# Kernel optimization log

Measured on AMD Instinct MI355X. Metric: run time of the kernel, lower is better.

The kernel has to match this reference:

```python
import math
import jax, jax.numpy as jnp
import numpy as np

B, T, E, H = 4, 2048, 256, 8
OBS_DIM, ACT_DIM = 17, 6
JOINED = OBS_DIM + ACT_DIM + 2  # 25: transition width in TAP trajectory transformer


def setup_inputs() -> dict:
    key = jax.random.key(0)
    ks = jax.random.split(key, 5)
    s = 0.02
    return {
        "x": jax.random.normal(ks[0], (B, T, E), dtype=jnp.float32),
        "Wq": jax.random.normal(ks[1], (E, E), dtype=jnp.float32) * s,
        "bq": jnp.zeros((E,), jnp.float32),
        "Wk": jax.random.normal(ks[2], (E, E), dtype=jnp.float32) * s,
        "bk": jnp.zeros((E,), jnp.float32),
        "Wv": jax.random.normal(ks[3], (E, E), dtype=jnp.float32) * s,
        "bv": jnp.zeros((E,), jnp.float32),
        "Wo": jax.random.normal(ks[4], (E, E), dtype=jnp.float32) * s,
        "bo": jnp.zeros((E,), jnp.float32),
    }


def _mask(t):
    # causal tril with every JOINED-th column (the "done"/boundary token) zeroed
    m = jnp.tril(jnp.ones((t, t), dtype=bool))
    keep_col = (jnp.arange(t) % JOINED) != (JOINED - 1)
    return m & keep_col[None, :]  # (t, t)


def reference(x, Wq, bq, Wk, bk, Wv, bv, Wo, bo):
    b, t, e = x.shape
    d = e // H
    # torch nn.Linear: y = x @ W.T + b
    q = (x @ Wq.T + bq).reshape(b, t, H, d).transpose(0, 2, 1, 3)  # b h t d
    k = (x @ Wk.T + bk).reshape(b, t, H, d).transpose(0, 2, 1, 3)
    v = (x @ Wv.T + bv).reshape(b, t, H, d).transpose(0, 2, 1, 3)

    scores = jnp.einsum("bhtd,bhsd->bhts", q, k) * (1.0 / math.sqrt(d))
    scores = jnp.where(_mask(t)[None, None], scores, -jnp.inf)
    attn = jax.nn.softmax(scores, axis=-1)  # (b, h, t, t) — dropout rate 0 => identity
    out = jnp.einsum("bhts,bhsd->bhtd", attn, v)  # b h t d
    out = out.transpose(0, 2, 1, 3).reshape(b, t, e)  # b t (h d)
    return out @ Wo.T + bo
```

## Files before the change

### kernel.cpp

```cpp
#include <hip/hip_runtime.h>

#define BB 4
#define TT 2048
#define EE 256
#define HH 8
#define DD 32
#define JOINED 25
#define CSCALE 0.2550539239731586f

typedef __attribute__((ext_vector_type(8))) __bf16 bf16x8;
typedef __attribute__((ext_vector_type(4))) float f32x4;

static __device__ __forceinline__ unsigned short f2bf(float f) {
    unsigned u = __float_as_uint(f);
    u += 0x7fffu + ((u >> 16) & 1u);
    return (unsigned short)(u >> 16);
}
static __device__ __forceinline__ unsigned pk2bf(float a, float b) {
    return (unsigned)f2bf(a) | ((unsigned)f2bf(b) << 16);
}

union BF8U { uint4 u; bf16x8 b; };
static __device__ __forceinline__ bf16x8 ld_frag(const unsigned short* p) {
    BF8U t; t.u = *(const uint4*)p; return t.b;
}

#define MFMA(a, b, c) __builtin_amdgcn_mfma_f32_16x16x32_bf16((a), (b), (c), 0, 0, 0)

__global__ __launch_bounds__(256) void prep_kernel(
    const float* __restrict__ x,
    const float* __restrict__ Wq, const float* __restrict__ Wk,
    const float* __restrict__ Wv, const float* __restrict__ Wo,
    unsigned short* __restrict__ xb, unsigned short* __restrict__ wqb,
    unsigned short* __restrict__ wkb, unsigned short* __restrict__ wvb,
    unsigned short* __restrict__ wob, unsigned short* __restrict__ onesG)
{
    const size_t NX = (size_t)BB * TT * EE;
    const size_t NMAIN = NX + 4 * (size_t)EE * EE;
    size_t idx = ((size_t)blockIdx.x * 256 + threadIdx.x) * 8;
    if (idx >= NMAIN) {
        size_t base = idx - NMAIN;
        #pragma unroll
        for (int i = 0; i < 8; ++i) {
            size_t e = base + i;
            if (e < (size_t)JOINED * 64) {
                int phase = (int)(e >> 6), o = (int)(e & 63);
                onesG[e] = (((phase + o) % JOINED) != (JOINED - 1)) ? (unsigned short)0x3F80
                                                                    : (unsigned short)0;
            }
        }
        return;
    }
    const float* src; unsigned short* dst; size_t off;
    if (idx < NX) { src = x; dst = xb; off = idx; }
    else {
        size_t i2 = idx - NX;
        int wsel = (int)(i2 >> 16);
        off = i2 & 65535u;
        src = wsel == 0 ? Wq : wsel == 1 ? Wk : wsel == 2 ? Wv : Wo;
        dst = wsel == 0 ? wqb : wsel == 1 ? wkb : wsel == 2 ? wvb : wob;
    }
    float4 a = *(const float4*)(src + off);
    float4 b = *(const float4*)(src + off + 4);
    uint4 o;
    o.x = pk2bf(a.x, a.y); o.y = pk2bf(a.z, a.w);
    o.z = pk2bf(b.x, b.y); o.w = pk2bf(b.z, b.w);
    *(uint4*)(dst + off) = o;
}

__global__ __launch_bounds__(256) void qkv_kernel(
    const unsigned short* __restrict__ xb,
    const unsigned short* __restrict__ wq, const float* __restrict__ bq,
    const unsigned short* __restrict__ wk, const float* __restrict__ bk,
    const unsigned short* __restrict__ wv, const float* __restrict__ bv,
    unsigned short* __restrict__ qo, unsigned short* __restrict__ ko,
    unsigned short* __restrict__ vto)
{
    __shared__ unsigned short Xs[64*72];
    __shared__ unsigned short Ws[64*72];

    const int m0 = blockIdx.x * 64;
    const int nb = blockIdx.y;
    const int which = nb >> 2;
    const int n0 = (nb & 3) * 64;
    const unsigned short* __restrict__ W = which == 0 ? wq : which == 1 ? wk : wv;
    const float* __restrict__ bias       = which == 0 ? bq : which == 1 ? bk : bv;

    const int tid = threadIdx.x;
    const int w = tid >> 6, lane = tid & 63, quad = lane >> 4, lq = lane & 15;
    const int sr = tid >> 2, sc = (tid & 3) * 16;

    f32x4 acc[4] = {{0,0,0,0},{0,0,0,0},{0,0,0,0},{0,0,0,0}};

    for (int k0 = 0; k0 < EE; k0 += 64) {
        __syncthreads();
        *(uint4*)&Xs[sr*72 + sc]     = *(const uint4*)&xb[(size_t)(m0 + sr)*EE + k0 + sc];
        *(uint4*)&Xs[sr*72 + sc + 8] = *(const uint4*)&xb[(size_t)(m0 + sr)*EE + k0 + sc + 8];
        *(uint4*)&Ws[sr*72 + sc]     = *(const uint4*)&W [(size_t)(n0 + sr)*EE + k0 + sc];
        *(uint4*)&Ws[sr*72 + sc + 8] = *(const uint4*)&W [(size_t)(n0 + sr)*EE + k0 + sc + 8];
        __syncthreads();
        bf16x8 a0 = ld_frag(&Xs[(w*16 + lq)*72 + quad*8]);
        bf16x8 a1 = ld_frag(&Xs[(w*16 + lq)*72 + 32 + quad*8]);
        #pragma unroll
        for (int f = 0; f < 4; ++f) {
            bf16x8 b0 = ld_frag(&Ws[(f*16 + lq)*72 + quad*8]);
            bf16x8 b1 = ld_frag(&Ws[(f*16 + lq)*72 + 32 + quad*8]);
            acc[f] = MFMA(a0, b0, acc[f]);
            acc[f] = MFMA(a1, b1, acc[f]);
        }
    }

    const int t0 = (m0 + w*16 + quad*4);
    const int b  = t0 >> 11;
    const int tl = t0 & (TT - 1);

    #pragma unroll
    for (int f = 0; f < 4; ++f) {
        int n = n0 + f*16 + lq;
        int h = n >> 5, d = n & 31;
        float bb = bias[n];
        if (which == 0) {
            #pragma unroll
            for (int reg = 0; reg < 4; ++reg)
                qo[(((size_t)b*HH + h)*TT + tl + reg)*DD + d] = f2bf((acc[f][reg] + bb) * CSCALE);
        } else if (which == 1) {
            #pragma unroll
            for (int reg = 0; reg < 4; ++reg)
                ko[(((size_t)b*HH + h)*TT + tl + reg)*DD + d] = f2bf(acc[f][reg] + bb);
        } else {
            int r25 = tl % JOINED;
            int mreg = (JOINED - 1) - r25;
            float vv[4];
            #pragma unroll
            for (int reg = 0; reg < 4; ++reg)
                vv[reg] = (reg == mreg) ? 0.f : (acc[f][reg] + bb);
            uint2 pk;
            pk.x = pk2bf(vv[0], vv[1]);
            pk.y = pk2bf(vv[2], vv[3]);
            *(uint2*)&vto[(((size_t)b*HH + h)*DD + d)*TT + tl] = pk;
        }
    }
}

__global__ __launch_bounds__(256, 4) void attn_kernel(
    const unsigned short* __restrict__ q, const unsigned short* __restrict__ k,
    const unsigned short* __restrict__ vt, const unsigned short* __restrict__ onesG,
    unsigned short* __restrict__ ao)
{
    __shared__ unsigned short Ks[2][64*40];
    __shared__ unsigned short Vt[2][32*72];
    __shared__ unsigned short Ps[4][16*72];

    const int L = blockIdx.x;
    const int xcd   = L & 7;
    const int inner = L >> 3;
    const int bh = xcd * 4 + (inner & 3);
    const int iq = 31 - (inner >> 2);
    const int b = bh >> 3, hh = bh & 7;

    const int tid = threadIdx.x;
    const int w = tid >> 6, lane = tid & 63, quad = lane >> 4, lq = lane & 15;
    const int r0 = iq * 64;
    const int q0 = r0 + w*16;
    const int ntiles = iq + 1;

    const int rk = tid >> 2, ck = (tid & 3) * 8;
    const int rv = tid >> 3, cv = (tid & 7) * 8;

    const unsigned short* qb_ = q  + (size_t)bh * TT * DD;
    const unsigned short* kb_ = k  + (size_t)bh * TT * DD;
    const unsigned short* vb_ = vt + (size_t)bh * DD * TT;

    const bf16x8 qf = ld_frag(qb_ + (size_t)(q0 + lq)*DD + quad*8);

    {
        uint4 kreg = *(const uint4*)(kb_ + (size_t)rk*DD + ck);
        uint4 vreg = *(const uint4*)(vb_ + (size_t)rv*TT + cv);
        *(uint4*)&Ks[0][rk*40 + ck] = kreg;
        *(uint4*)&Vt[0][rv*72 + cv] = vreg;
    }
    __syncthreads();

    f32x4 O0 = {0,0,0,0}, O1 = {0,0,0,0}, Ld = {0,0,0,0};
    int phase = 0;

    for (int jt = 0; jt < ntiles; ++jt) {
        const int j0 = jt * 64;
        const int jn = (jt + 1 < ntiles) ? j0 + 64 : j0;
        uint4 kreg = *(const uint4*)(kb_ + (size_t)(jn + rk)*DD + ck);
        uint4 vreg = *(const uint4*)(vb_ + (size_t)rv*TT + jn + cv);

        bf16x8 ones0 = ld_frag(&onesG[phase*64 +      quad*8]);
        bf16x8 ones1 = ld_frag(&onesG[phase*64 + 32 + quad*8]);

        const unsigned short* Kb = &Ks[jt & 1][0];
        const unsigned short* Vb = &Vt[jt & 1][0];

        f32x4 St[4];
        #pragma unroll
        for (int f = 0; f < 4; ++f) {
            bf16x8 kf = ld_frag(&Kb[(f*16 + lq)*40 + quad*8]);
            f32x4 z = {0,0,0,0};
            St[f] = MFMA(kf, qf, z);
        }
        if (jt == ntiles - 1) {
            int row = q0 + lq;
            #pragma unroll
            for (int f = 0; f < 4; ++f) {
                int kvb = j0 + f*16 + quad*4;
                #pragma unroll
                for (int reg = 0; reg < 4; ++reg)
                    St[f][reg] = (kvb + reg <= row) ? St[f][reg] : -1e30f;
            }
        }
        unsigned short* ps = &Ps[w][0];
        #pragma unroll
        for (int f = 0; f < 4; ++f) {
            float p0 = __builtin_amdgcn_exp2f(St[f][0]);
            float p1 = __builtin_amdgcn_exp2f(St[f][1]);
            float p2 = __builtin_amdgcn_exp2f(St[f][2]);
            float p3 = __builtin_amdgcn_exp2f(St[f][3]);
            uint2 pk;
            pk.x = pk2bf(p0, p1);
            pk.y = pk2bf(p2, p3);
            *(uint2*)&ps[lq*72 + f*16 + quad*4] = pk;
        }
        #pragma unroll
        for (int c = 0; c < 2; ++c) {
            bf16x8 pa  = ld_frag(&ps[lq*72 + c*32 + quad*8]);
            bf16x8 v0f = ld_frag(&Vb[(lq)*72      + c*32 + quad*8]);
            bf16x8 v1f = ld_frag(&Vb[(16 + lq)*72 + c*32 + quad*8]);
            O0 = MFMA(pa, v0f, O0);
            O1 = MFMA(pa, v1f, O1);
            Ld = MFMA(pa, (c ? ones1 : ones0), Ld);
        }

        *(uint4*)&Ks[(jt + 1) & 1][rk*40 + ck] = kreg;
        *(uint4*)&Vt[(jt + 1) & 1][rv*72 + cv] = vreg;
        __syncthreads();

        phase += 14; if (phase >= JOINED) phase -= JOINED;
    }

    #pragma unroll
    for (int reg = 0; reg < 4; ++reg) {
        float inv = 1.0f / Ld[reg];
        int t = q0 + quad*4 + reg;
        size_t ob = ((size_t)b*TT + t)*EE + hh*DD;
        ao[ob + lq]      = f2bf(O0[reg] * inv);
        ao[ob + 16 + lq] = f2bf(O1[reg] * inv);
    }
}

__global__ __launch_bounds__(256) void proj_kernel(
    const unsigned short* __restrict__ a, const unsigned short* __restrict__ W,
    const float* __restrict__ bias, float* __restrict__ out)
{
    __shared__ unsigned short Xs[64*72];
    __shared__ unsigned short Ws[64*72];

    const int m0 = blockIdx.x * 64;
    const int n0 = blockIdx.y * 64;
    const int tid = threadIdx.x;
    const int w = tid >> 6, lane = tid & 63, quad = lane >> 4, lq = lane & 15;
    const int sr = tid >> 2, sc = (tid & 3) * 16;

    f32x4 acc[4] = {{0,0,0,0},{0,0,0,0},{0,0,0,0},{0,0,0,0}};

    for (int k0 = 0; k0 < EE; k0 += 64) {
        __syncthreads();
        *(uint4*)&Xs[sr*72 + sc]     = *(const uint4*)&a[(size_t)(m0 + sr)*EE + k0 + sc];
        *(uint4*)&Xs[sr*72 + sc + 8] = *(const uint4*)&a[(size_t)(m0 + sr)*EE + k0 + sc + 8];
        *(uint4*)&Ws[sr*72 + sc]     = *(const uint4*)&W[(size_t)(n0 + sr)*EE + k0 + sc];
        *(uint4*)&Ws[sr*72 + sc + 8] = *(const uint4*)&W[(size_t)(n0 + sr)*EE + k0 + sc + 8];
        __syncthreads();
        bf16x8 a0 = ld_frag(&Xs[(w*16 + lq)*72 + quad*8]);
        bf16x8 a1 = ld_frag(&Xs[(w*16 + lq)*72 + 32 + quad*8]);
        #pragma unroll
        for (int f = 0; f < 4; ++f) {
            bf16x8 b0 = ld_frag(&Ws[(f*16 + lq)*72 + quad*8]);
            bf16x8 b1 = ld_frag(&Ws[(f*16 + lq)*72 + 32 + quad*8]);
            acc[f] = MFMA(a0, b0, acc[f]);
            acc[f] = MFMA(a1, b1, acc[f]);
        }
    }

    #pragma unroll
    for (int f = 0; f < 4; ++f) {
        int n = n0 + f*16 + lq;
        float bb = bias[n];
        #pragma unroll
        for (int reg = 0; reg < 4; ++reg) {
            int m = m0 + w*16 + quad*4 + reg;
            out[(size_t)m*EE + n] = acc[f][reg] + bb;
        }
    }
}

extern "C" void kernel_launch(void* const* d_in, const int* in_sizes, int n_in,
                              void* d_out, int out_size, void* d_ws, size_t ws_size,
                              hipStream_t stream) {
    const float* x  = (const float*)d_in[0];
    const float* Wq = (const float*)d_in[1];
    const float* bq = (const float*)d_in[2];
    const float* Wk = (const float*)d_in[3];
    const float* bk = (const float*)d_in[4];
    const float* Wv = (const float*)d_in[5];
    const float* bv = (const float*)d_in[6];
    const float* Wo = (const float*)d_in[7];
    const float* bo = (const float*)d_in[8];
    float* out = (float*)d_out;

    const size_t n_elem = (size_t)BB * TT * EE;
    const size_t w_elem = (size_t)EE * EE;
    unsigned short* xb    = (unsigned short*)d_ws;
    unsigned short* wqb   = xb  + n_elem;
    unsigned short* wkb   = wqb + w_elem;
    unsigned short* wvb   = wkb + w_elem;
    unsigned short* wob   = wvb + w_elem;
    unsigned short* qq    = wob + w_elem;
    unsigned short* kk    = qq  + n_elem;
    unsigned short* vtt   = kk  + n_elem;
    unsigned short* ao    = vtt + n_elem;
    unsigned short* onesG = ao  + n_elem;

    const int prep_blocks = (int)((n_elem + 4*w_elem) / 2048) + 1;
    prep_kernel<<<dim3(prep_blocks), 256, 0, stream>>>(
        x, Wq, Wk, Wv, Wo, xb, wqb, wkb, wvb, wob, onesG);
    qkv_kernel <<<dim3(BB*TT/64, 12), 256, 0, stream>>>(
        xb, wqb, bq, wkb, bk, wvb, bv, qq, kk, vtt);
    attn_kernel<<<dim3(1024), 256, 0, stream>>>(qq, kk, vtt, onesG, ao);
    proj_kernel<<<dim3(BB*TT/64, EE/64), 256, 0, stream>>>(ao, wob, bo, out);
}
```

Baseline: 120.1 us.

## Use 128-row query tiles with 512-thread blocks and in-LDS ones table

The attention kernel now handles 128 query rows per block with 8 waves. Each K/V tile is loaded into shared memory once and reused by twice as many query rows, and half the threads stage K while the other half stage V. Waves skip key tiles that lie entirely beyond their causal horizon. The boundary-mask ones table is built in LDS inside the attention kernel rather than by prep_kernel in global memory. The cost is fewer blocks, larger blocks, and some idle waves near the causal diagonal.

```diff
diff --git a/kernel.cpp b/kernel.cpp
--- a/kernel.cpp
+++ b/kernel.cpp
@@ -33,24 +33,10 @@
     const float* __restrict__ Wv, const float* __restrict__ Wo,
     unsigned short* __restrict__ xb, unsigned short* __restrict__ wqb,
     unsigned short* __restrict__ wkb, unsigned short* __restrict__ wvb,
-    unsigned short* __restrict__ wob, unsigned short* __restrict__ onesG)
+    unsigned short* __restrict__ wob)
 {
     const size_t NX = (size_t)BB * TT * EE;
-    const size_t NMAIN = NX + 4 * (size_t)EE * EE;
     size_t idx = ((size_t)blockIdx.x * 256 + threadIdx.x) * 8;
-    if (idx >= NMAIN) {
-        size_t base = idx - NMAIN;
-        #pragma unroll
-        for (int i = 0; i < 8; ++i) {
-            size_t e = base + i;
-            if (e < (size_t)JOINED * 64) {
-                int phase = (int)(e >> 6), o = (int)(e & 63);
-                onesG[e] = (((phase + o) % JOINED) != (JOINED - 1)) ? (unsigned short)0x3F80
-                                                                    : (unsigned short)0;
-            }
-        }
-        return;
-    }
     const float* src; unsigned short* dst; size_t off;
     if (idx < NX) { src = x; dst = xb; off = idx; }
     else {
@@ -142,30 +128,38 @@
     }
 }
 
-__global__ __launch_bounds__(256, 4) void attn_kernel(
+__global__ __launch_bounds__(512, 2) void attn_kernel(
     const unsigned short* __restrict__ q, const unsigned short* __restrict__ k,
-    const unsigned short* __restrict__ vt, const unsigned short* __restrict__ onesG,
-    unsigned short* __restrict__ ao)
+    const unsigned short* __restrict__ vt, unsigned short* __restrict__ ao)
 {
     __shared__ unsigned short Ks[2][64*40];
     __shared__ unsigned short Vt[2][32*72];
-    __shared__ unsigned short Ps[4][16*72];
+    __shared__ unsigned short Ps[8][16*72];
+    __shared__ unsigned short onesTab[JOINED*64];
 
     const int L = blockIdx.x;
     const int xcd   = L & 7;
     const int inner = L >> 3;
     const int bh = xcd * 4 + (inner & 3);
-    const int iq = 31 - (inner >> 2);
+    const int iq = 15 - (inner >> 2);
     const int b = bh >> 3, hh = bh & 7;
 
     const int tid = threadIdx.x;
     const int w = tid >> 6, lane = tid & 63, quad = lane >> 4, lq = lane & 15;
-    const int r0 = iq * 64;
+    const int r0 = iq * 128;
     const int q0 = r0 + w*16;
-    const int ntiles = iq + 1;
-
-    const int rk = tid >> 2, ck = (tid & 3) * 8;
-    const int rv = tid >> 3, cv = (tid & 7) * 8;
+    const int ntiles = iq*2 + 2;
+
+    const bool stK = tid < 256;
+    const int t2 = tid & 255;
+    const int rk = t2 >> 2, ck = (t2 & 3) * 8;
+    const int rv = t2 >> 3, cv = (t2 & 7) * 8;
+
+    for (int i = tid; i < JOINED*64; i += 512) {
+        int phase = i >> 6, o = i & 63;
+        onesTab[i] = (((phase + o) % JOINED) != (JOINED - 1)) ? (unsigned short)0x3F80
+                                                              : (unsigned short)0;
+    }
 
     const unsigned short* qb_ = q  + (size_t)bh * TT * DD;
     const unsigned short* kb_ = k  + (size_t)bh * TT * DD;
@@ -173,12 +167,8 @@
 
     const bf16x8 qf = ld_frag(qb_ + (size_t)(q0 + lq)*DD + quad*8);
 
-    {
-        uint4 kreg = *(const uint4*)(kb_ + (size_t)rk*DD + ck);
-        uint4 vreg = *(const uint4*)(vb_ + (size_t)rv*TT + cv);
-        *(uint4*)&Ks[0][rk*40 + ck] = kreg;
-        *(uint4*)&Vt[0][rv*72 + cv] = vreg;
-    }
+    if (stK) *(uint4*)&Ks[0][rk*40 + ck] = *(const uint4*)(kb_ + (size_t)rk*DD + ck);
+    else     *(uint4*)&Vt[0][rv*72 + cv] = *(const uint4*)(vb_ + (size_t)rv*TT + cv);
     __syncthreads();
 
     f32x4 O0 = {0,0,0,0}, O1 = {0,0,0,0}, Ld = {0,0,0,0};
@@ -187,56 +177,59 @@
     for (int jt = 0; jt < ntiles; ++jt) {
         const int j0 = jt * 64;
         const int jn = (jt + 1 < ntiles) ? j0 + 64 : j0;
-        uint4 kreg = *(const uint4*)(kb_ + (size_t)(jn + rk)*DD + ck);
-        uint4 vreg = *(const uint4*)(vb_ + (size_t)rv*TT + jn + cv);
-
-        bf16x8 ones0 = ld_frag(&onesG[phase*64 +      quad*8]);
-        bf16x8 ones1 = ld_frag(&onesG[phase*64 + 32 + quad*8]);
-
-        const unsigned short* Kb = &Ks[jt & 1][0];
-        const unsigned short* Vb = &Vt[jt & 1][0];
-
-        f32x4 St[4];
-        #pragma unroll
-        for (int f = 0; f < 4; ++f) {
-            bf16x8 kf = ld_frag(&Kb[(f*16 + lq)*40 + quad*8]);
-            f32x4 z = {0,0,0,0};
-            St[f] = MFMA(kf, qf, z);
-        }
-        if (jt == ntiles - 1) {
-            int row = q0 + lq;
+        uint4 sreg;
+        if (stK) sreg = *(const uint4*)(kb_ + (size_t)(jn + rk)*DD + ck);
+        else     sreg = *(const uint4*)(vb_ + (size_t)rv*TT + jn + cv);
+
+        if (j0 <= q0 + 15) {
+            const unsigned short* Kb = &Ks[jt & 1][0];
+            const unsigned short* Vb = &Vt[jt & 1][0];
+
+            bf16x8 ones0 = ld_frag(&onesTab[phase*64 +      quad*8]);
+            bf16x8 ones1 = ld_frag(&onesTab[phase*64 + 32 + quad*8]);
+
+            f32x4 St[4];
             #pragma unroll
             for (int f = 0; f < 4; ++f) {
-                int kvb = j0 + f*16 + quad*4;
+                bf16x8 kf = ld_frag(&Kb[(f*16 + lq)*40 + quad*8]);
+                f32x4 z = {0,0,0,0};
+                St[f] = MFMA(kf, qf, z);
+            }
+            if (j0 + 63 > q0) {
+                int row = q0 + lq;
                 #pragma unroll
-                for (int reg = 0; reg < 4; ++reg)
-                    St[f][reg] = (kvb + reg <= row) ? St[f][reg] : -1e30f;
+                for (int f = 0; f < 4; ++f) {
+                    int kvb = j0 + f*16 + quad*4;
+                    #pragma unroll
+                    for (int reg = 0; reg < 4; ++reg)
+                        St[f][reg] = (kvb + reg <= row) ? St[f][reg] : -1e30f;
+                }
             }
-        }
-        unsigned short* ps = &Ps[w][0];
-        #pragma unroll
-        for (int f = 0; f < 4; ++f) {
-            float p0 = __builtin_amdgcn_exp2f(St[f][0]);
-            float p1 = __builtin_amdgcn_exp2f(St[f][1]);
-            float p2 = __builtin_amdgcn_exp2f(St[f][2]);
-            float p3 = __builtin_amdgcn_exp2f(St[f][3]);
-            uint2 pk;
-            pk.x = pk2bf(p0, p1);
-            pk.y = pk2bf(p2, p3);
-            *(uint2*)&ps[lq*72 + f*16 + quad*4] = pk;
-        }
-        #pragma unroll
-        for (int c = 0; c < 2; ++c) {
-            bf16x8 pa  = ld_frag(&ps[lq*72 + c*32 + quad*8]);
-            bf16x8 v0f = ld_frag(&Vb[(lq)*72      + c*32 + quad*8]);
-            bf16x8 v1f = ld_frag(&Vb[(16 + lq)*72 + c*32 + quad*8]);
-            O0 = MFMA(pa, v0f, O0);
-            O1 = MFMA(pa, v1f, O1);
-            Ld = MFMA(pa, (c ? ones1 : ones0), Ld);
-        }
-
-        *(uint4*)&Ks[(jt + 1) & 1][rk*40 + ck] = kreg;
-        *(uint4*)&Vt[(jt + 1) & 1][rv*72 + cv] = vreg;
+            unsigned short* ps = &Ps[w][0];
+            #pragma unroll
+            for (int f = 0; f < 4; ++f) {
+                float p0 = __builtin_amdgcn_exp2f(St[f][0]);
+                float p1 = __builtin_amdgcn_exp2f(St[f][1]);
+                float p2 = __builtin_amdgcn_exp2f(St[f][2]);
+                float p3 = __builtin_amdgcn_exp2f(St[f][3]);
+                uint2 pk;
+                pk.x = pk2bf(p0, p1);
+                pk.y = pk2bf(p2, p3);
+                *(uint2*)&ps[lq*72 + f*16 + quad*4] = pk;
+            }
+            #pragma unroll
+            for (int c = 0; c < 2; ++c) {
+                bf16x8 pa  = ld_frag(&ps[lq*72 + c*32 + quad*8]);
+                bf16x8 v0f = ld_frag(&Vb[(lq)*72      + c*32 + quad*8]);
+                bf16x8 v1f = ld_frag(&Vb[(16 + lq)*72 + c*32 + quad*8]);
+                O0 = MFMA(pa, v0f, O0);
+                O1 = MFMA(pa, v1f, O1);
+                Ld = MFMA(pa, (c ? ones1 : ones0), Ld);
+            }
+        }
+
+        if (stK) *(uint4*)&Ks[(jt + 1) & 1][rk*40 + ck] = sreg;
+        else     *(uint4*)&Vt[(jt + 1) & 1][rv*72 + cv] = sreg;
         __syncthreads();
 
         phase += 14; if (phase >= JOINED) phase -= JOINED;
@@ -322,13 +315,12 @@
     unsigned short* kk    = qq  + n_elem;
     unsigned short* vtt   = kk  + n_elem;
     unsigned short* ao    = vtt + n_elem;
-    unsigned short* onesG = ao  + n_elem;
-
-    const int prep_blocks = (int)((n_elem + 4*w_elem) / 2048) + 1;
+
+    const int prep_blocks = (int)((n_elem + 4*w_elem) / 2048);
     prep_kernel<<<dim3(prep_blocks), 256, 0, stream>>>(
-        x, Wq, Wk, Wv, Wo, xb, wqb, wkb, wvb, wob, onesG);
+        x, Wq, Wk, Wv, Wo, xb, wqb, wkb, wvb, wob);
     qkv_kernel <<<dim3(BB*TT/64, 12), 256, 0, stream>>>(
         xb, wqb, bq, wkb, bk, wvb, bv, qq, kk, vtt);
-    attn_kernel<<<dim3(1024), 256, 0, stream>>>(qq, kk, vtt, onesG, ao);
+    attn_kernel<<<dim3(512), 512, 0, stream>>>(qq, kk, vtt, ao);
     proj_kernel<<<dim3(BB*TT/64, EE/64), 256, 0, stream>>>(ao, wob, bo, out);
 }
```

New measurement: 126.2 us. +5.1%, slower.
